# Performance work log

Measured on AMD Instinct MI355X. Metric: run time of the kernel, lower is better.

The kernel has to match this reference:

```python
import jax, jax.numpy as jnp
import numpy as np

EMB = 256
D_INNER = 512                         # expand=2 * d_model
HEADDIM = 64
NHEADS = D_INNER // HEADDIM           # 8
DSTATE = 128
DCONV = 4
CONV_DIM = D_INNER + 2 * DSTATE       # 768 (ngroups=1)
D_IN_PROJ = 2 * D_INNER + 2 * DSTATE + NHEADS  # 1288
LN_EPS = 1e-5


def _layernorm(x, w, b):
    m = jnp.mean(x, axis=-1, keepdims=True)
    v = jnp.mean((x - m) ** 2, axis=-1, keepdims=True)
    return (x - m) * jax.lax.rsqrt(v + LN_EPS) * w + b


def _wn_linear(x, g, v, b):
    # torch weight_norm(dim=0): w = g * v / ||v|| per output row
    w = g[:, None] * v / jnp.linalg.norm(v, axis=1, keepdims=True)
    return x @ w.T + b


def _ssm_scan(x, dt, A, Bm, Cm):
    # x: (b,l,h,p)  dt: (b,l,h)  A: (h,)  Bm/Cm: (b,l,n)
    dA = jnp.exp(dt * A)           # (b,l,h), A<0 so dA in (0,1)
    dtx = dt[..., None] * x        # (b,l,h,p)
    bsz = x.shape[0]

    def step(h, inp):
        dA_t, dtx_t, B_t, C_t = inp
        h = h * dA_t[:, :, None, None] + dtx_t[..., None] * B_t[:, None, None, :]
        y = jnp.einsum('bhpn,bn->bhp', h, C_t)
        return h, y

    h0 = jnp.zeros((bsz, NHEADS, HEADDIM, DSTATE), x.dtype)
    xs = (jnp.swapaxes(dA, 0, 1), jnp.swapaxes(dtx, 0, 1),
          jnp.swapaxes(Bm, 0, 1), jnp.swapaxes(Cm, 0, 1))
    _, ys = jax.lax.scan(step, h0, xs)
    return jnp.swapaxes(ys, 0, 1)  # (b,l,h,p)


def _mamba2(u, in_proj_w, conv_w, conv_b, dt_bias, A_log, D_param, ssm_norm_w, out_proj_w):
    B, L, _ = u.shape
    zxbcdt = u @ in_proj_w.T                       # (B,L,1288)
    z_gate = zxbcdt[..., :D_INNER]
    xBC = zxbcdt[..., D_INNER:D_INNER + CONV_DIM]
    dt = zxbcdt[..., D_INNER + CONV_DIM:]
    # causal depthwise conv1d
    xp = jnp.pad(xBC, ((0, 0), (DCONV - 1, 0), (0, 0)))
    xc = jax.lax.conv_general_dilated(
        jnp.swapaxes(xp, 1, 2), conv_w[:, None, :], (1,), 'VALID',
        feature_group_count=CONV_DIM, dimension_numbers=('NCH', 'OIH', 'NCH'))
    xc = jax.nn.silu(jnp.swapaxes(xc, 1, 2) + conv_b)
    x = xc[..., :D_INNER].reshape(B, L, NHEADS, HEADDIM)
    Bm = xc[..., D_INNER:D_INNER + DSTATE]
    Cm = xc[..., D_INNER + DSTATE:]
    dt = jax.nn.softplus(dt + dt_bias)             # (B,L,H)
    A = -jnp.exp(A_log)                            # (H,)
    y = _ssm_scan(x, dt, A, Bm, Cm) + D_param[None, None, :, None] * x
    y = y.reshape(B, L, D_INNER)
    # gated RMSNorm (norm_before_gate=False): rmsnorm(y * silu(z)) * w
    yg = y * jax.nn.silu(z_gate)
    yn = yg * jax.lax.rsqrt(jnp.mean(yg ** 2, axis=-1, keepdims=True) + LN_EPS) * ssm_norm_w
    return yn @ out_proj_w.T


def setup_inputs() -> dict:
    key = jax.random.key(0)
    ks = jax.random.split(key, 12)
    B, NU, NA = 1, 64, 512

    def rn(k, shape, scale):
        return jax.random.normal(k, shape, dtype=jnp.float32) * scale

    z = rn(ks[0], (B, NU, NA, EMB), 1.0)
    in_proj_w = rn(ks[1], (D_IN_PROJ, EMB), EMB ** -0.5)
    conv_w = rn(ks[2], (CONV_DIM, DCONV), DCONV ** -0.5)
    conv_b = rn(ks[3], (CONV_DIM,), 0.02)
    dt_bias = jnp.log(jnp.expm1(jax.random.uniform(ks[4], (NHEADS,), minval=0.001, maxval=0.1)))
    A_log = jnp.log(jax.random.uniform(ks[5], (NHEADS,), minval=1.0, maxval=16.0))
    D_param = jnp.ones((NHEADS,), dtype=jnp.float32)
    ssm_norm_w = jnp.ones((D_INNER,), dtype=jnp.float32)
    out_proj_w = rn(ks[6], (EMB, D_INNER), D_INNER ** -0.5)
    ff_v = rn(ks[7], (EMB, EMB), EMB ** -0.5)
    ff_g = jnp.linalg.norm(ff_v, axis=1)
    ff_b = jnp.zeros((EMB,), dtype=jnp.float32)
    fc1_v = rn(ks[8], (EMB, EMB), EMB ** -0.5)
    fc1_g = jnp.linalg.norm(fc1_v, axis=1)
    fc1_b = jnp.zeros((EMB,), dtype=jnp.float32)
    fc2_v = rn(ks[9], (EMB, EMB), EMB ** -0.5)
    fc2_g = jnp.linalg.norm(fc2_v, axis=1)
    fc2_b = jnp.zeros((EMB,), dtype=jnp.float32)
    return {
        'z': z,
        'ln1_w': jnp.ones((EMB,), dtype=jnp.float32), 'ln1_b': jnp.zeros((EMB,), dtype=jnp.float32),
        'in_proj_w': in_proj_w, 'conv_w': conv_w, 'conv_b': conv_b,
        'dt_bias': dt_bias, 'A_log': A_log, 'D_param': D_param,
        'ssm_norm_w': ssm_norm_w, 'out_proj_w': out_proj_w,
        'ff_g': ff_g, 'ff_v': ff_v, 'ff_b': ff_b,
        'ln2_w': jnp.ones((EMB,), dtype=jnp.float32), 'ln2_b': jnp.zeros((EMB,), dtype=jnp.float32),
        'fc1_g': fc1_g, 'fc1_v': fc1_v, 'fc1_b': fc1_b,
        'fc2_g': fc2_g, 'fc2_v': fc2_v, 'fc2_b': fc2_b,
    }


def reference(z, ln1_w, ln1_b, in_proj_w, conv_w, conv_b, dt_bias, A_log, D_param,
              ssm_norm_w, out_proj_w, ff_g, ff_v, ff_b, ln2_w, ln2_b,
              fc1_g, fc1_v, fc1_b, fc2_g, fc2_v, fc2_b):
    b, nu, na, e = z.shape
    # MambaBlock: z + ff(mamba(norm(z)))
    u = _layernorm(z, ln1_w, ln1_b).reshape(-1, na, e)
    y = _mamba2(u, in_proj_w, conv_w, conv_b, dt_bias, A_log, D_param, ssm_norm_w, out_proj_w)
    y = _wn_linear(y, ff_g, ff_v, ff_b).reshape(b, nu, na, e)
    z = z + y
    # NormFF: z + Lin2(GELU(Lin1(LN(z))))  (dropout inactive in eval)
    h = _layernorm(z, ln2_w, ln2_b)
    h = jax.nn.gelu(_wn_linear(h, fc1_g, fc1_v, fc1_b), approximate=False)
    h = _wn_linear(h, fc2_g, fc2_v, fc2_b)
    return z + h
```

## Files before the change

### kernel.cpp

```cpp
#include <hip/hip_runtime.h>
#include <stdint.h>
#include <math.h>

#define EMB       256
#define D_INNER   512
#define HEADDIM   64
#define NHEADS    8
#define DSTATE    128
#define DCONV     4
#define CONV_DIM  768
#define LN_EPS    1e-5f
#define NBATCH    64
#define SEQLEN    512
#define NTOK      (NBATCH*SEQLEN)

typedef __attribute__((ext_vector_type(8))) short          short8;
typedef __attribute__((ext_vector_type(8))) unsigned short u16x8;
typedef __attribute__((ext_vector_type(4))) unsigned short u16x4;
typedef __attribute__((ext_vector_type(4))) float          f32x4;

__device__ __forceinline__ float bfb(unsigned short u) {
    union { unsigned int i; float f; } x; x.i = ((unsigned int)u) << 16; return x.f;
}
__device__ __forceinline__ unsigned short fbf(float f) {
    union { float f; unsigned int i; } x; x.f = f;
    unsigned int i = x.i;
    unsigned int lsb = (i >> 16) & 1u;
    i += 0x7fffu + lsb;
    return (unsigned short)(i >> 16);
}

__device__ __forceinline__ void gld16(const unsigned short* g, unsigned short* l) {
    __builtin_amdgcn_global_load_lds((const __attribute__((address_space(1))) void*)g,
                                     (__attribute__((address_space(3))) void*)l, 16, 0, 0);
}

__global__ __launch_bounds__(256) void cvt2_k(const float* __restrict__ a, unsigned short* __restrict__ oa, int na,
                                              const float* __restrict__ b, unsigned short* __restrict__ ob, int nb) {
    int i = blockIdx.x * 256 + threadIdx.x;
    if (i < na) oa[i] = fbf(a[i]);
    else { i -= na; if (i < nb) ob[i] = fbf(b[i]); }
}

__global__ __launch_bounds__(256) void wnorm3_k(const float* __restrict__ g0, const float* __restrict__ v0, unsigned short* __restrict__ o0,
                                                const float* __restrict__ g1, const float* __restrict__ v1, unsigned short* __restrict__ o1,
                                                const float* __restrict__ g2, const float* __restrict__ v2, unsigned short* __restrict__ o2) {
    int o = blockIdx.x & 255, s = blockIdx.x >> 8, tid = threadIdx.x;
    const float* g = s == 0 ? g0 : (s == 1 ? g1 : g2);
    const float* v = s == 0 ? v0 : (s == 1 ? v1 : v2);
    unsigned short* wout = s == 0 ? o0 : (s == 1 ? o1 : o2);
    float x = v[(size_t)o * 256 + tid];
    float q = x * x;
    __shared__ float sm[4];
    #pragma unroll
    for (int d = 32; d; d >>= 1) q += __shfl_down(q, d);
    if ((tid & 63) == 0) sm[tid >> 6] = q;
    __syncthreads();
    float tot = sm[0] + sm[1] + sm[2] + sm[3];
    float scale = g[o] * rsqrtf(tot);
    wout[(size_t)o * 256 + tid] = fbf(x * scale);
}

__global__ __launch_bounds__(256) void wco_k(const unsigned short* __restrict__ wff,
                                             const unsigned short* __restrict__ outWb,
                                             unsigned short* __restrict__ wco) {
    int i = blockIdx.x, tid = threadIdx.x;
    __shared__ float row[256];
    row[tid] = bfb(wff[(size_t)i * 256 + tid]);
    __syncthreads();
    #pragma unroll
    for (int half = 0; half < 2; half++) {
        int k = tid + half * 256;
        float acc = 0.f;
        for (int j = 0; j < 256; j++)
            acc += row[j] * bfb(outWb[(size_t)j * 512 + k]);
        wco[(size_t)i * 512 + k] = fbf(acc);
    }
}

__global__ __launch_bounds__(256) void ln_k(const float* __restrict__ in,
                                            const float* __restrict__ w,
                                            const float* __restrict__ b,
                                            unsigned short* __restrict__ out) {
    int tok = blockIdx.x, tid = threadIdx.x;
    size_t idx = (size_t)tok * 256 + tid;
    float x = in[idx];
    __shared__ float sm[8];
    float s = x;
    #pragma unroll
    for (int o = 32; o; o >>= 1) s += __shfl_down(s, o);
    if ((tid & 63) == 0) sm[tid >> 6] = s;
    __syncthreads();
    float mean = (sm[0] + sm[1] + sm[2] + sm[3]) * (1.f / 256.f);
    float d = x - mean;
    float q = d * d;
    #pragma unroll
    for (int o = 32; o; o >>= 1) q += __shfl_down(q, o);
    if ((tid & 63) == 0) sm[4 + (tid >> 6)] = q;
    __syncthreads();
    float var = (sm[4] + sm[5] + sm[6] + sm[7]) * (1.f / 256.f);
    out[idx] = fbf(d * rsqrtf(var + LN_EPS) * w[tid] + b[tid]);
}

#define BMT 128
#define BNT 128
#define BKT 32
template<int EPI, int NBN>
__global__ __launch_bounds__(256) void gemm_k(const unsigned short* __restrict__ A,
                                              const unsigned short* __restrict__ Bw,
                                              int K, int N,
                                              unsigned short* __restrict__ out_b,
                                              float* __restrict__ out_f,
                                              const float* __restrict__ bias,
                                              const float* __restrict__ res_f,
                                              unsigned short* __restrict__ out2_b) {
    __shared__ __align__(16) unsigned short smem[16384];
    int tid = threadIdx.x;
    int d = blockIdx.x;
    const int cpx = (256 * NBN) >> 3;
    int logical = (d & 7) * cpx + (d >> 3);
    int bm = logical / NBN;
    int bn = logical % NBN;
    int lane = tid & 63, w = tid >> 6;
    int wr = w >> 1, wc = w & 1;
    int fr = lane & 15, fq = lane >> 4;

    int rsub = w * 16 + (lane >> 2);
    int cl   = ((lane & 3) ^ ((rsub >> 1) & 3)) << 3;
    const unsigned short* gA0 = A  + (size_t)(bm * BMT + rsub)      * K + cl;
    const unsigned short* gA1 = A  + (size_t)(bm * BMT + rsub + 64) * K + cl;
    const unsigned short* gB0 = Bw + (size_t)(bn * BNT + rsub)      * K + cl;
    const unsigned short* gB1 = Bw + (size_t)(bn * BNT + rsub + 64) * K + cl;

    f32x4 acc[4][4];
    #pragma unroll
    for (int m = 0; m < 4; m++)
        #pragma unroll
        for (int n = 0; n < 4; n++)
            #pragma unroll
            for (int r = 0; r < 4; r++) acc[m][n][r] = 0.f;

    auto AS = [&](int buf) { return &smem[buf * 4096]; };
    auto BS = [&](int buf) { return &smem[8192 + buf * 4096]; };
    auto STAGE = [&](int buf, int k0) {
        gld16(gA0 + k0, AS(buf) + w * 512);
        gld16(gA1 + k0, AS(buf) + 2048 + w * 512);
        gld16(gB0 + k0, BS(buf) + w * 512);
        gld16(gB1 + k0, BS(buf) + 2048 + w * 512);
    };

    int nt = K / BKT;
    STAGE(0, 0);
    STAGE(1, BKT);
    for (int t = 0; t < nt; ++t) {
        int buf = t & 1;
        if (t < nt - 1) asm volatile("s_waitcnt vmcnt(4)" ::: "memory");
        else            asm volatile("s_waitcnt vmcnt(0)" ::: "memory");
        __builtin_amdgcn_s_barrier();
        short8 af[4], bf_[4];
        #pragma unroll
        for (int m = 0; m < 4; m++) {
            int ra = wr * 64 + m * 16 + fr;
            af[m] = *(const short8*)&AS(buf)[ra * 32 + ((fq ^ ((ra >> 1) & 3)) << 3)];
        }
        #pragma unroll
        for (int n = 0; n < 4; n++) {
            int rb = wc * 64 + n * 16 + fr;
            bf_[n] = *(const short8*)&BS(buf)[rb * 32 + ((fq ^ ((rb >> 1) & 3)) << 3)];
        }
        asm volatile("s_waitcnt lgkmcnt(0)" ::: "memory");
        __builtin_amdgcn_sched_barrier(0);
        __builtin_amdgcn_s_barrier();
        if (t + 2 < nt) STAGE(buf, (t + 2) * BKT);
        __builtin_amdgcn_s_setprio(1);
        #pragma unroll
        for (int m = 0; m < 4; m++)
            #pragma unroll
            for (int n = 0; n < 4; n++)
                acc[m][n] = __builtin_amdgcn_mfma_f32_16x16x32_bf16(af[m], bf_[n], acc[m][n], 0, 0, 0);
        __builtin_amdgcn_s_setprio(0);
    }
    __builtin_amdgcn_s_barrier();

    if (EPI == 1 && bn == 10) {
        #pragma unroll
        for (int m = 0; m < 4; m++)
            #pragma unroll
            for (int n = 0; n < 4; n++)
                #pragma unroll
                for (int r = 0; r < 4; r++) {
                    int grow = bm * BMT + wr * 64 + m * 16 + fq * 4 + r;
                    int gcol = 1280 + wc * 64 + n * 16 + fr;
                    if (gcol < 1288) {
                        float a2 = acc[m][n][r] + bias[gcol - 1280];
                        out_f[(size_t)grow * 8 + (gcol - 1280)] =
                            a2 > 20.f ? a2 : log1pf(expf(a2));
                    }
                }
    } else if (EPI == 0 || EPI == 1) {
        unsigned short* cb = smem;
        #pragma unroll
        for (int s = 0; s < 2; s++) {
            if (wr == s) {
                #pragma unroll
                for (int m = 0; m < 4; m++)
                    #pragma unroll
                    for (int n = 0; n < 4; n++)
                        #pragma unroll
                        for (int r = 0; r < 4; r++)
                            cb[(m * 16 + fq * 4 + r) * 136 + wc * 64 + n * 16 + fr] =
                                fbf(acc[m][n][r]);
            }
            __syncthreads();
            #pragma unroll
            for (int k = 0; k < 4; k++) {
                int g = k * 256 + tid;
                int row = g >> 4, col = (g & 15) << 3;
                u16x8 v = *(const u16x8*)&cb[row * 136 + col];
                int grow = bm * BMT + s * 64 + row;
                int gc = bn * BNT + col;
                if (EPI == 0) {
                    *(u16x8*)&out_b[(size_t)grow * N + gc] = v;
                } else {
                    if (gc < 512) *(u16x8*)&out_b[(size_t)grow * 512 + gc] = v;
                    else          *(u16x8*)&out2_b[(size_t)grow * 768 + (gc - 512)] = v;
                }
            }
            __syncthreads();
        }
    } else {
        float* fb = (float*)smem;
        #pragma unroll
        for (int s = 0; s < 4; s++) {
            if (wr == (s >> 1)) {
                int mp = s & 1;
                #pragma unroll
                for (int mm = 0; mm < 2; mm++)
                    #pragma unroll
                    for (int n = 0; n < 4; n++)
                        #pragma unroll
                        for (int r = 0; r < 4; r++)
                            fb[(mm * 16 + fq * 4 + r) * 132 + wc * 64 + n * 16 + fr] =
                                acc[mp * 2 + mm][n][r];
            }
            __syncthreads();
            #pragma unroll
            for (int k = 0; k < 4; k++) {
                int g = k * 256 + tid;
                int row = g >> 5, col = (g & 31) << 2;
                f32x4 v = *(const f32x4*)&fb[row * 132 + col];
                int grow = bm * BMT + (s >> 1) * 64 + (s & 1) * 32 + row;
                int gc = bn * BNT + col;
                size_t idx = (size_t)grow * 256 + gc;
                if (EPI == 2) {
                    f32x4 rr = *(const f32x4*)&res_f[idx];
                    f32x4 o;
                    #pragma unroll
                    for (int j = 0; j < 4; j++) o[j] = rr[j] + v[j] + bias[gc + j];
                    *(f32x4*)&out_f[idx] = o;
                } else {
                    u16x4 o;
                    #pragma unroll
                    for (int j = 0; j < 4; j++) {
                        float x = v[j] + bias[gc + j];
                        o[j] = fbf(0.5f * x * (1.f + erff(x * 0.70710678118654752f)));
                    }
                    *(u16x4*)&out_b[idx] = o;
                }
            }
            __syncthreads();
        }
    }
}

__global__ __launch_bounds__(256) void conv_k(unsigned short* xbc,
                                              const float* __restrict__ cw,
                                              const float* __restrict__ cb) {
    int b = blockIdx.y;
    int c0 = blockIdx.x * 64;
    int tid = threadIdx.x;
    int c = tid & 63;
    int rq = tid >> 6;
    __shared__ unsigned short sraw[131][72];
    int ca = c0 + c;
    float w0 = cw[ca * 4 + 0], w1 = cw[ca * 4 + 1];
    float w2 = cw[ca * 4 + 2], w3 = cw[ca * 4 + 3];
    float bias = cb[ca];
    unsigned short carry_u = 0;

    for (int t0 = 0; t0 < 512; t0 += 128) {
        __syncthreads();
        if (tid < 192) sraw[rq][c] = carry_u;
        for (int idx = tid; idx < 1024; idx += 256) {
            int lt = idx >> 3, cg = idx & 7;
            *(u16x8*)&sraw[3 + lt][cg * 8] =
                *(const u16x8*)&xbc[((size_t)(b * 512 + t0 + lt)) * 768 + c0 + cg * 8];
        }
        __syncthreads();
        if (tid < 192) carry_u = sraw[128 + rq][c];
        #pragma unroll 4
        for (int i = 0; i < 32; i++) {
            int lt = rq + 4 * i;
            float acc = bias
                + bfb(sraw[lt + 0][c]) * w0
                + bfb(sraw[lt + 1][c]) * w1
                + bfb(sraw[lt + 2][c]) * w2
                + bfb(sraw[lt + 3][c]) * w3;
            acc = acc / (1.f + expf(-acc));
            xbc[((size_t)(b * 512 + t0 + lt)) * 768 + c0 + c] = fbf(acc);
        }
    }
}

#define CPAD 136
#define TPAD 56
#define TOFF(r) ((((r) >> 4) & 3) << 3)
__global__ __launch_bounds__(256) void ssd_k(const unsigned short* __restrict__ xc,
                                             const float* __restrict__ dts,
                                             const float* __restrict__ A_log,
                                             const float* __restrict__ D_param,
                                             unsigned short* __restrict__ y) {
    __shared__ unsigned short Ct[32][CPAD];
    __shared__ unsigned short Bt[32][CPAD];
    __shared__ unsigned short BtT[128][TPAD];
    __shared__ unsigned short DXT[64][TPAD];
    __shared__ unsigned short LG[32][40];
    __shared__ unsigned short hB[64][CPAD];
    __shared__ unsigned short Yb[32][72];
    __shared__ float scum[32], sdt2[32], sEC[32];
    __shared__ float sET[32][36];

    int bh = blockIdx.x;
    int b = bh >> 3, h = bh & 7;
    int tid = threadIdx.x;
    int w = tid >> 6;
    int lane = tid & 63;
    int fr = lane & 15, fq = lane >> 4;

    float A_h = -expf(A_log[h]);
    float D_h = D_param[h];

    f32x4 hacc[8];
    #pragma unroll
    for (int nf = 0; nf < 8; nf++)
        #pragma unroll
        for (int r = 0; r < 4; r++) hacc[nf][r] = 0.f;

    int t  = tid >> 3;
    int e8 = tid & 7;

    for (int c = 0; c < 16; ++c) {
        size_t tok0 = (size_t)b * 512 + c * 32;
        u16x8 bv0, bv1, cv0, cv1, xv;
        {
            const unsigned short* row = &xc[(tok0 + t) * 768];
            bv0 = *(const u16x8*)&row[512 + e8 * 16];
            bv1 = *(const u16x8*)&row[512 + e8 * 16 + 8];
            cv0 = *(const u16x8*)&row[640 + e8 * 16];
            cv1 = *(const u16x8*)&row[640 + e8 * 16 + 8];
            xv  = *(const u16x8*)&row[h * 64 + e8 * 8];
        }
        *(u16x8*)&Ct[t][e8 * 16]     = cv0;
        *(u16x8*)&Ct[t][e8 * 16 + 8] = cv1;
        *(u16x8*)&Bt[t][e8 * 16]     = bv0;
        *(u16x8*)&Bt[t][e8 * 16 + 8] = bv1;
        if (tid < 32) {
            float dtv = dts[(tok0 + tid) * 8 + h];
            sdt2[tid] = dtv;
            float la = dtv * A_h;
            #pragma unroll
            for (int dd = 1; dd < 32; dd <<= 1) {
                float up = __shfl_up(la, dd);
                if (lane >= dd) la += up;
            }
            scum[tid] = la;
        }
        __syncthreads();
        float cumQ = scum[31];
        if (tid < 32) sEC[tid] = expf(scum[tid]);
        {
            float dtv = sdt2[t];
            float wgt = expf(cumQ - scum[t]);
            int tof = TOFF(e8 * 16);
            #pragma unroll
            for (int j = 0; j < 8; j++) {
                float dtx = dtv * bfb(xv[j]);
                int rr = e8 * 8 + j;
                DXT[rr][t + TOFF(rr)] = fbf(dtx);
                BtT[e8 * 16 + j][t + tof]     = fbf(wgt * bfb(bv0[j]));
                BtT[e8 * 16 + 8 + j][t + tof] = fbf(wgt * bfb(bv1[j]));
            }
        }
        #pragma unroll
        for (int k = 0; k < 4; k++) {
            int idx = tid * 4 + k;
            int tt = idx >> 5, tq = idx & 31;
            sET[tt][tq] = (tq <= tt) ? expf(scum[tt] - scum[tq]) : 0.f;
        }
        #pragma unroll
        for (int nf = 0; nf < 8; nf++)
            #pragma unroll
            for (int r = 0; r < 4; r++)
                hB[w * 16 + fq * 4 + r][nf * 16 + fr] = fbf(hacc[nf][r]);
        __syncthreads();
        {
            int m = w >> 1, nf = w & 1;
            f32x4 g;
            #pragma unroll
            for (int r = 0; r < 4; r++) g[r] = 0.f;
            #pragma unroll
            for (int ks = 0; ks < 4; ks++) {
                short8 ca = *(const short8*)&Ct[m * 16 + fr][ks * 32 + fq * 8];
                short8 bb = *(const short8*)&Bt[nf * 16 + fr][ks * 32 + fq * 8];
                g = __builtin_amdgcn_mfma_f32_16x16x32_bf16(ca, bb, g, 0, 0, 0);
            }
            #pragma unroll
            for (int r = 0; r < 4; r++) {
                int tt = m * 16 + fq * 4 + r;
                int tq = nf * 16 + fr;
                LG[tt][tq] = fbf(g[r] * sET[tt][tq]);
            }
        }
        __syncthreads();
        f32x4 Yi[2];
        #pragma unroll
        for (int m = 0; m < 2; m++)
            #pragma unroll
            for (int r = 0; r < 4; r++) Yi[m][r] = 0.f;
        #pragma unroll
        for (int ks = 0; ks < 4; ks++) {
            short8 a0 = *(const short8*)&Ct[fr][ks * 32 + fq * 8];
            short8 a1 = *(const short8*)&Ct[16 + fr][ks * 32 + fq * 8];
            short8 hb = *(const short8*)&hB[w * 16 + fr][ks * 32 + fq * 8];
            Yi[0] = __builtin_amdgcn_mfma_f32_16x16x32_bf16(a0, hb, Yi[0], 0, 0, 0);
            Yi[1] = __builtin_amdgcn_mfma_f32_16x16x32_bf16(a1, hb, Yi[1], 0, 0, 0);
        }
        #pragma unroll
        for (int m = 0; m < 2; m++)
            #pragma unroll
            for (int r = 0; r < 4; r++) Yi[m][r] *= sEC[m * 16 + fq * 4 + r];
        {
            int wof = TOFF(w * 16);
            short8 a0 = *(const short8*)&LG[fr][fq * 8];
            short8 a1 = *(const short8*)&LG[16 + fr][fq * 8];
            short8 dx = *(const short8*)&DXT[w * 16 + fr][fq * 8 + wof];
            Yi[0] = __builtin_amdgcn_mfma_f32_16x16x32_bf16(a0, dx, Yi[0], 0, 0, 0);
            Yi[1] = __builtin_amdgcn_mfma_f32_16x16x32_bf16(a1, dx, Yi[1], 0, 0, 0);
        }
        {
            float ecq = sEC[31];
            #pragma unroll
            for (int nf = 0; nf < 8; nf++)
                #pragma unroll
                for (int r = 0; r < 4; r++) hacc[nf][r] *= ecq;
            int wof = TOFF(w * 16);
            short8 ax = *(const short8*)&DXT[w * 16 + fr][fq * 8 + wof];
            #pragma unroll
            for (int nf = 0; nf < 8; nf++) {
                short8 bb = *(const short8*)&BtT[nf * 16 + fr][fq * 8 + TOFF(nf * 16)];
                hacc[nf] = __builtin_amdgcn_mfma_f32_16x16x32_bf16(ax, bb, hacc[nf], 0, 0, 0);
            }
        }
        #pragma unroll
        for (int m = 0; m < 2; m++)
            #pragma unroll
            for (int r = 0; r < 4; r++) {
                int tt = m * 16 + fq * 4 + r;
                Yb[tt][w * 16 + fr] = fbf(Yi[m][r]);
            }
        __syncthreads();
        {
            u16x8 yv = *(const u16x8*)&Yb[t][e8 * 8];
            u16x8 ov;
            #pragma unroll
            for (int j = 0; j < 8; j++)
                ov[j] = fbf(bfb(yv[j]) + D_h * bfb(xv[j]));
            *(u16x8*)&y[(tok0 + t) * 512 + h * 64 + e8 * 8] = ov;
        }
    }
}

__global__ __launch_bounds__(256) void gate_k(const unsigned short* __restrict__ y,
                                              const unsigned short* __restrict__ zg,
                                              const float* __restrict__ nw,
                                              unsigned short* __restrict__ yn) {
    int tok = blockIdx.x, tid = threadIdx.x;
    size_t base = (size_t)tok * 512;
    float gv[2];
    float q = 0.f;
    #pragma unroll
    for (int j = 0; j < 2; j++) {
        int c = tid + j * 256;
        float yy = bfb(y[base + c]);
        float zz = bfb(zg[base + c]);
        float s = zz / (1.f + expf(-zz));
        float t = yy * s;
        gv[j] = t;
        q += t * t;
    }
    __shared__ float sm[4];
    #pragma unroll
    for (int o = 32; o; o >>= 1) q += __shfl_down(q, o);
    if ((tid & 63) == 0) sm[tid >> 6] = q;
    __syncthreads();
    float ms = (sm[0] + sm[1] + sm[2] + sm[3]) * (1.f / 512.f);
    float r = rsqrtf(ms + LN_EPS);
    #pragma unroll
    for (int j = 0; j < 2; j++) {
        int c = tid + j * 256;
        yn[base + c] = fbf(gv[j] * r * nw[c]);
    }
}

extern "C" void kernel_launch(void* const* d_in, const int* in_sizes, int n_in,
                              void* d_out, int out_size, void* d_ws, size_t ws_size,
                              hipStream_t stream) {
    if (n_in < 22) return;
    static const int setup_sizes[22] = {8388608,256,256,329728,3072,768,8,8,8,512,
                                        131072,256,65536,256,256,256,256,65536,256,256,65536,256};
    for (int i = 0; i < 22; i++) if (in_sizes[i] != setup_sizes[i]) return;

    const float* z      = (const float*)d_in[0];
    const float* ln1w   = (const float*)d_in[1];
    const float* ln1b   = (const float*)d_in[2];
    const float* inW    = (const float*)d_in[3];
    const float* convw  = (const float*)d_in[4];
    const float* convb  = (const float*)d_in[5];
    const float* dtb    = (const float*)d_in[6];
    const float* Alog   = (const float*)d_in[7];
    const float* Dp     = (const float*)d_in[8];
    const float* normw  = (const float*)d_in[9];
    const float* outW   = (const float*)d_in[10];
    const float* ffg    = (const float*)d_in[11];
    const float* ffv    = (const float*)d_in[12];
    const float* ffb    = (const float*)d_in[13];
    const float* ln2w   = (const float*)d_in[14];
    const float* ln2b   = (const float*)d_in[15];
    const float* fc1g   = (const float*)d_in[16];
    const float* fc1v   = (const float*)d_in[17];
    const float* fc1b   = (const float*)d_in[18];
    const float* fc2g   = (const float*)d_in[19];
    const float* fc2v   = (const float*)d_in[20];
    const float* fc2b   = (const float*)d_in[21];
    float* out = (float*)d_out;
    (void)out_size;

    char* ws = (char*)d_ws;
    const size_t SLOT_A = (size_t)NTOK * 768 * 2;
    const size_t SLOT_B = (size_t)NTOK * 512 * 2;
    const size_t SLOT_C = (size_t)NTOK * 512 * 2;
    const size_t SLOT_D = (size_t)NTOK * 256 * 2;
    const size_t SLOT_E = (size_t)NTOK * 8 * 4;
    const size_t SLOT_W = (size_t)256 * 256 * 2;
    const size_t SLOT_WI = (size_t)1288 * 256 * 2;
    const size_t SLOT_WO = (size_t)256 * 512 * 2;
    const size_t SLOT_WC = (size_t)256 * 512 * 2;
    char* pA = ws;
    char* pB = pA + SLOT_A;
    char* pC = pB + SLOT_B;
    char* pD = pC + SLOT_C;
    char* pE = pD + SLOT_D;
    char* pW = pE + SLOT_E;
    char* pWI = pW + 3 * SLOT_W;
    char* pWO = pWI + SLOT_WI;
    char* pWC = pWO + SLOT_WO;
    size_t need = SLOT_A + SLOT_B + SLOT_C + SLOT_D + SLOT_E + 3 * SLOT_W + SLOT_WI + SLOT_WO + SLOT_WC;
    if (ws_size < need) return;

    unsigned short* xbc = (unsigned short*)pA;
    unsigned short* yn  = (unsigned short*)pA;
    unsigned short* t2  = (unsigned short*)(pA + (size_t)NTOK * 512 * 2);
    unsigned short* y   = (unsigned short*)pB;
    float*          z2  = (float*)pB;
    unsigned short* zgb = (unsigned short*)pC;
    unsigned short* u   = (unsigned short*)pD;
    unsigned short* h1  = (unsigned short*)pD;
    float*          dts = (float*)pE;
    unsigned short* wff  = (unsigned short*)pW;
    unsigned short* wfc1 = (unsigned short*)(pW + SLOT_W);
    unsigned short* wfc2 = (unsigned short*)(pW + 2 * SLOT_W);
    unsigned short* inWb = (unsigned short*)pWI;
    unsigned short* outWb = (unsigned short*)pWO;
    unsigned short* wco  = (unsigned short*)pWC;

    cvt2_k<<<(1288 * 256 + 131072 + 255) / 256, 256, 0, stream>>>(inW, inWb, 1288 * 256,
                                                                  outW, outWb, 131072);
    wnorm3_k<<<768, 256, 0, stream>>>(ffg, ffv, wff, fc1g, fc1v, wfc1, fc2g, fc2v, wfc2);
    wco_k<<<256, 256, 0, stream>>>(wff, outWb, wco);
    ln_k<<<NTOK, 256, 0, stream>>>(z, ln1w, ln1b, u);
    gemm_k<1, 11><<<256 * 11, 256, 0, stream>>>(u, inWb, 256, 1288,
                                                zgb, dts, dtb, nullptr, xbc);
    conv_k<<<dim3(12, 64), 256, 0, stream>>>(xbc, convw, convb);
    ssd_k<<<NBATCH * NHEADS, 256, 0, stream>>>(xbc, dts, Alog, Dp, y);
    gate_k<<<NTOK, 256, 0, stream>>>(y, zgb, normw, yn);
    gemm_k<2, 2><<<256 * 2, 256, 0, stream>>>(yn, wco, 512, 256,
                                              nullptr, z2, ffb, z, nullptr);
    ln_k<<<NTOK, 256, 0, stream>>>(z2, ln2w, ln2b, t2);
    gemm_k<3, 2><<<256 * 2, 256, 0, stream>>>(t2, wfc1, 256, 256,
                                              h1, nullptr, fc1b, nullptr, nullptr);
    gemm_k<2, 2><<<256 * 2, 256, 0, stream>>>(h1, wfc2, 256, 256,
                                              nullptr, out, fc2b, z2, nullptr);
}
```

Before: 317.6 us.

## Parallelize causal conv over time chunks using halo rows written by in-proj GEMM

The in-projection GEMM epilogue now also writes the last three pre-conv rows of each 128-token chunk into a separate halo buffer. This lets the conv kernel run each chunk independently, with a 3D grid of 4 chunks per batch instead of a serial carry loop over time, which raises parallelism fourfold. The GEMM also takes K as a compile-time template parameter so the loop count is constant, and its launch bounds request 3 waves per SIMD for occupancy. The cost is extra workspace, extra conditional stores in the GEMM epilogue, and a small extra halo read in the conv.

Result: slower. 336.8 us (+6.0%).

```diff
diff --git a/kernel.cpp b/kernel.cpp
--- a/kernel.cpp
+++ b/kernel.cpp
@@ -105,15 +105,16 @@
 #define BMT 128
 #define BNT 128
 #define BKT 32
-template<int EPI, int NBN>
-__global__ __launch_bounds__(256) void gemm_k(const unsigned short* __restrict__ A,
-                                              const unsigned short* __restrict__ Bw,
-                                              int K, int N,
-                                              unsigned short* __restrict__ out_b,
-                                              float* __restrict__ out_f,
-                                              const float* __restrict__ bias,
-                                              const float* __restrict__ res_f,
-                                              unsigned short* __restrict__ out2_b) {
+template<int EPI, int NBN, int KT>
+__global__ __launch_bounds__(256, 3) void gemm_k(const unsigned short* __restrict__ A,
+                                                 const unsigned short* __restrict__ Bw,
+                                                 int N,
+                                                 unsigned short* __restrict__ out_b,
+                                                 float* __restrict__ out_f,
+                                                 const float* __restrict__ bias,
+                                                 const float* __restrict__ res_f,
+                                                 unsigned short* __restrict__ out2_b,
+                                                 unsigned short* __restrict__ halo) {
     __shared__ __align__(16) unsigned short smem[16384];
     int tid = threadIdx.x;
     int d = blockIdx.x;
@@ -127,10 +128,8 @@
 
     int rsub = w * 16 + (lane >> 2);
     int cl   = ((lane & 3) ^ ((rsub >> 1) & 3)) << 3;
-    const unsigned short* gA0 = A  + (size_t)(bm * BMT + rsub)      * K + cl;
-    const unsigned short* gA1 = A  + (size_t)(bm * BMT + rsub + 64) * K + cl;
-    const unsigned short* gB0 = Bw + (size_t)(bn * BNT + rsub)      * K + cl;
-    const unsigned short* gB1 = Bw + (size_t)(bn * BNT + rsub + 64) * K + cl;
+    const unsigned short* gA0 = A  + (size_t)(bm * BMT + rsub) * KT + cl;
+    const unsigned short* gB0 = Bw + (size_t)(bn * BNT + rsub) * KT + cl;
 
     f32x4 acc[4][4];
     #pragma unroll
@@ -144,12 +143,12 @@
     auto BS = [&](int buf) { return &smem[8192 + buf * 4096]; };
     auto STAGE = [&](int buf, int k0) {
         gld16(gA0 + k0, AS(buf) + w * 512);
-        gld16(gA1 + k0, AS(buf) + 2048 + w * 512);
+        gld16(gA0 + k0 + (size_t)64 * KT, AS(buf) + 2048 + w * 512);
         gld16(gB0 + k0, BS(buf) + w * 512);
-        gld16(gB1 + k0, BS(buf) + 2048 + w * 512);
+        gld16(gB0 + k0 + (size_t)64 * KT, BS(buf) + 2048 + w * 512);
     };
 
-    int nt = K / BKT;
+    constexpr int nt = KT / BKT;
     STAGE(0, 0);
     STAGE(1, BKT);
     for (int t = 0; t < nt; ++t) {
@@ -223,7 +222,13 @@
                     *(u16x8*)&out_b[(size_t)grow * N + gc] = v;
                 } else {
                     if (gc < 512) *(u16x8*)&out_b[(size_t)grow * 512 + gc] = v;
-                    else          *(u16x8*)&out2_b[(size_t)grow * 768 + (gc - 512)] = v;
+                    else {
+                        *(u16x8*)&out2_b[(size_t)grow * 768 + (gc - 512)] = v;
+                        int tr = grow & 127;
+                        int H  = grow >> 7;
+                        if (tr >= 125 && (H & 3) != 3)
+                            *(u16x8*)&halo[((size_t)(H + 1) * 3 + (tr - 125)) * 768 + (gc - 512)] = v;
+                    }
                 }
             }
             __syncthreads();
@@ -274,41 +279,44 @@
 }
 
 __global__ __launch_bounds__(256) void conv_k(unsigned short* xbc,
+                                              const unsigned short* __restrict__ halo,
                                               const float* __restrict__ cw,
                                               const float* __restrict__ cb) {
-    int b = blockIdx.y;
+    int b  = blockIdx.y;
+    int c  = blockIdx.z;
     int c0 = blockIdx.x * 64;
+    int t0 = c * 128;
     int tid = threadIdx.x;
-    int c = tid & 63;
-    int rq = tid >> 6;
+    int cth = tid & 63;
+    int rq  = tid >> 6;
     __shared__ unsigned short sraw[131][72];
-    int ca = c0 + c;
+
+    int ca = c0 + cth;
     float w0 = cw[ca * 4 + 0], w1 = cw[ca * 4 + 1];
     float w2 = cw[ca * 4 + 2], w3 = cw[ca * 4 + 3];
     float bias = cb[ca];
-    unsigned short carry_u = 0;
-
-    for (int t0 = 0; t0 < 512; t0 += 128) {
-        __syncthreads();
-        if (tid < 192) sraw[rq][c] = carry_u;
-        for (int idx = tid; idx < 1024; idx += 256) {
-            int lt = idx >> 3, cg = idx & 7;
-            *(u16x8*)&sraw[3 + lt][cg * 8] =
-                *(const u16x8*)&xbc[((size_t)(b * 512 + t0 + lt)) * 768 + c0 + cg * 8];
-        }
-        __syncthreads();
-        if (tid < 192) carry_u = sraw[128 + rq][c];
-        #pragma unroll 4
-        for (int i = 0; i < 32; i++) {
-            int lt = rq + 4 * i;
-            float acc = bias
-                + bfb(sraw[lt + 0][c]) * w0
-                + bfb(sraw[lt + 1][c]) * w1
-                + bfb(sraw[lt + 2][c]) * w2
-                + bfb(sraw[lt + 3][c]) * w3;
-            acc = acc / (1.f + expf(-acc));
-            xbc[((size_t)(b * 512 + t0 + lt)) * 768 + c0 + c] = fbf(acc);
-        }
+
+    if (tid < 192) {
+        int j = tid >> 6, cc = tid & 63;
+        sraw[j][cc] = (c == 0) ? (unsigned short)0
+            : halo[((size_t)(b * 4 + c) * 3 + j) * 768 + c0 + cc];
+    }
+    for (int idx = tid; idx < 1024; idx += 256) {
+        int lt = idx >> 3, cg = idx & 7;
+        *(u16x8*)&sraw[3 + lt][cg * 8] =
+            *(const u16x8*)&xbc[((size_t)(b * 512 + t0 + lt)) * 768 + c0 + cg * 8];
+    }
+    __syncthreads();
+    #pragma unroll 4
+    for (int i = 0; i < 32; i++) {
+        int lt = rq + 4 * i;
+        float acc = bias
+            + bfb(sraw[lt + 0][cth]) * w0
+            + bfb(sraw[lt + 1][cth]) * w1
+            + bfb(sraw[lt + 2][cth]) * w2
+            + bfb(sraw[lt + 3][cth]) * w3;
+        acc = acc / (1.f + expf(-acc));
+        xbc[((size_t)(b * 512 + t0 + lt)) * 768 + c0 + cth] = fbf(acc);
     }
 }
 
@@ -555,6 +563,7 @@
     const size_t SLOT_WI = (size_t)1288 * 256 * 2;
     const size_t SLOT_WO = (size_t)256 * 512 * 2;
     const size_t SLOT_WC = (size_t)256 * 512 * 2;
+    const size_t SLOT_H  = (size_t)256 * 3 * 768 * 2;
     char* pA = ws;
     char* pB = pA + SLOT_A;
     char* pC = pB + SLOT_B;
@@ -564,7 +573,8 @@
     char* pWI = pW + 3 * SLOT_W;
     char* pWO = pWI + SLOT_WI;
     char* pWC = pWO + SLOT_WO;
-    size_t need = SLOT_A + SLOT_B + SLOT_C + SLOT_D + SLOT_E + 3 * SLOT_W + SLOT_WI + SLOT_WO + SLOT_WC;
+    char* pH  = pWC + SLOT_WC;
+    size_t need = SLOT_A + SLOT_B + SLOT_C + SLOT_D + SLOT_E + 3 * SLOT_W + SLOT_WI + SLOT_WO + SLOT_WC + SLOT_H;
     if (ws_size < need) return;
 
     unsigned short* xbc = (unsigned short*)pA;
@@ -582,22 +592,23 @@
     unsigned short* inWb = (unsigned short*)pWI;
     unsigned short* outWb = (unsigned short*)pWO;
     unsigned short* wco  = (unsigned short*)pWC;
+    unsigned short* halo = (unsigned short*)pH;
 
     cvt2_k<<<(1288 * 256 + 131072 + 255) / 256, 256, 0, stream>>>(inW, inWb, 1288 * 256,
                                                                   outW, outWb, 131072);
     wnorm3_k<<<768, 256, 0, stream>>>(ffg, ffv, wff, fc1g, fc1v, wfc1, fc2g, fc2v, wfc2);
     wco_k<<<256, 256, 0, stream>>>(wff, outWb, wco);
     ln_k<<<NTOK, 256, 0, stream>>>(z, ln1w, ln1b, u);
-    gemm_k<1, 11><<<256 * 11, 256, 0, stream>>>(u, inWb, 256, 1288,
-                                                zgb, dts, dtb, nullptr, xbc);
-    conv_k<<<dim3(12, 64), 256, 0, stream>>>(xbc, convw, convb);
+    gemm_k<1, 11, 256><<<256 * 11, 256, 0, stream>>>(u, inWb, 1288,
+                                                     zgb, dts, dtb, nullptr, xbc, halo);
+    conv_k<<<dim3(12, 64, 4), 256, 0, stream>>>(xbc, halo, convw, convb);
     ssd_k<<<NBATCH * NHEADS, 256, 0, stream>>>(xbc, dts, Alog, Dp, y);
     gate_k<<<NTOK, 256, 0, stream>>>(y, zgb, normw, yn);
-    gemm_k<2, 2><<<256 * 2, 256, 0, stream>>>(yn, wco, 512, 256,
-                                              nullptr, z2, ffb, z, nullptr);
+    gemm_k<2, 2, 512><<<256 * 2, 256, 0, stream>>>(yn, wco, 256,
+                                                   nullptr, z2, ffb, z, nullptr, nullptr);
     ln_k<<<NTOK, 256, 0, stream>>>(z2, ln2w, ln2b, t2);
-    gemm_k<3, 2><<<256 * 2, 256, 0, stream>>>(t2, wfc1, 256, 256,
-                                              h1, nullptr, fc1b, nullptr, nullptr);
-    gemm_k<2, 2><<<256 * 2, 256, 0, stream>>>(h1, wfc2, 256, 256,
-                                              nullptr, out, fc2b, z2, nullptr);
-}
+    gemm_k<3, 2, 256><<<256 * 2, 256, 0, stream>>>(t2, wfc1, 256,
+                                                   h1, nullptr, fc1b, nullptr, nullptr, nullptr);
+    gemm_k<2, 2, 256><<<256 * 2, 256, 0, stream>>>(h1, wfc2, 256,
+                                                   nullptr, out, fc2b, z2, nullptr, nullptr);
+}
```

## Split causal conv across time chunks with halo buffer; prefetch SSD inputs

Applied to the files above, without the earlier changes.

A new halo kernel copies the three boundary rows before each 128-token chunk into a side buffer. The conv kernel can then run one block per chunk, giving 4x more blocks instead of a serial loop over chunks per block. The SSD kernel remaps block indices so that heads of the same batch group are spread across blocks, and it prefetches the next chunk's B/C/x rows into registers before the barrier to hide global load latency. The cost is an extra kernel launch, more workspace, and higher register pressure in ssd_k.

Measured after the change: 308.6 us. -2.8%, faster.

```diff
diff --git a/kernel.cpp b/kernel.cpp
--- a/kernel.cpp
+++ b/kernel.cpp
@@ -273,42 +273,58 @@
     }
 }
 
+__global__ __launch_bounds__(256) void halo_k(const unsigned short* __restrict__ xbc,
+                                              unsigned short* __restrict__ halo) {
+    int blk = blockIdx.x;
+    int b = blk / 3, c = blk % 3 + 1;
+    int tid = threadIdx.x;
+    for (int i = tid; i < 288; i += 256) {
+        int j = i / 96, off = (i % 96) * 8;
+        size_t tok = (size_t)b * 512 + c * 128 - 3 + j;
+        *(u16x8*)&halo[((size_t)(b * 4 + c) * 3 + j) * 768 + off] =
+            *(const u16x8*)&xbc[tok * 768 + off];
+    }
+}
+
 __global__ __launch_bounds__(256) void conv_k(unsigned short* xbc,
+                                              const unsigned short* __restrict__ halo,
                                               const float* __restrict__ cw,
                                               const float* __restrict__ cb) {
-    int b = blockIdx.y;
+    int b  = blockIdx.y;
+    int c  = blockIdx.z;
     int c0 = blockIdx.x * 64;
+    int t0 = c * 128;
     int tid = threadIdx.x;
-    int c = tid & 63;
-    int rq = tid >> 6;
+    int cth = tid & 63;
+    int rq  = tid >> 6;
     __shared__ unsigned short sraw[131][72];
-    int ca = c0 + c;
+
+    int ca = c0 + cth;
     float w0 = cw[ca * 4 + 0], w1 = cw[ca * 4 + 1];
     float w2 = cw[ca * 4 + 2], w3 = cw[ca * 4 + 3];
     float bias = cb[ca];
-    unsigned short carry_u = 0;
-
-    for (int t0 = 0; t0 < 512; t0 += 128) {
-        __syncthreads();
-        if (tid < 192) sraw[rq][c] = carry_u;
-        for (int idx = tid; idx < 1024; idx += 256) {
-            int lt = idx >> 3, cg = idx & 7;
-            *(u16x8*)&sraw[3 + lt][cg * 8] =
-                *(const u16x8*)&xbc[((size_t)(b * 512 + t0 + lt)) * 768 + c0 + cg * 8];
-        }
-        __syncthreads();
-        if (tid < 192) carry_u = sraw[128 + rq][c];
-        #pragma unroll 4
-        for (int i = 0; i < 32; i++) {
-            int lt = rq + 4 * i;
-            float acc = bias
-                + bfb(sraw[lt + 0][c]) * w0
-                + bfb(sraw[lt + 1][c]) * w1
-                + bfb(sraw[lt + 2][c]) * w2
-                + bfb(sraw[lt + 3][c]) * w3;
-            acc = acc / (1.f + expf(-acc));
-            xbc[((size_t)(b * 512 + t0 + lt)) * 768 + c0 + c] = fbf(acc);
-        }
+
+    if (tid < 192) {
+        int j = tid >> 6, cc = tid & 63;
+        sraw[j][cc] = (c == 0) ? (unsigned short)0
+            : halo[((size_t)(b * 4 + c) * 3 + j) * 768 + c0 + cc];
+    }
+    for (int idx = tid; idx < 1024; idx += 256) {
+        int lt = idx >> 3, cg = idx & 7;
+        *(u16x8*)&sraw[3 + lt][cg * 8] =
+            *(const u16x8*)&xbc[((size_t)(b * 512 + t0 + lt)) * 768 + c0 + cg * 8];
+    }
+    __syncthreads();
+    #pragma unroll 4
+    for (int i = 0; i < 32; i++) {
+        int lt = rq + 4 * i;
+        float acc = bias
+            + bfb(sraw[lt + 0][cth]) * w0
+            + bfb(sraw[lt + 1][cth]) * w1
+            + bfb(sraw[lt + 2][cth]) * w2
+            + bfb(sraw[lt + 3][cth]) * w3;
+        acc = acc / (1.f + expf(-acc));
+        xbc[((size_t)(b * 512 + t0 + lt)) * 768 + c0 + cth] = fbf(acc);
     }
 }
 
@@ -330,8 +346,9 @@
     __shared__ float scum[32], sdt2[32], sEC[32];
     __shared__ float sET[32][36];
 
-    int bh = blockIdx.x;
-    int b = bh >> 3, h = bh & 7;
+    int d = blockIdx.x;
+    int b = (d & 7) | (((d >> 6) & 7) << 3);
+    int h = (d >> 3) & 7;
     int tid = threadIdx.x;
     int w = tid >> 6;
     int lane = tid & 63;
@@ -349,17 +366,18 @@
     int t  = tid >> 3;
     int e8 = tid & 7;
 
+    u16x8 bv0, bv1, cv0, cv1, xv;
+    {
+        const unsigned short* row = &xc[((size_t)b * 512 + t) * 768];
+        bv0 = *(const u16x8*)&row[512 + e8 * 16];
+        bv1 = *(const u16x8*)&row[512 + e8 * 16 + 8];
+        cv0 = *(const u16x8*)&row[640 + e8 * 16];
+        cv1 = *(const u16x8*)&row[640 + e8 * 16 + 8];
+        xv  = *(const u16x8*)&row[h * 64 + e8 * 8];
+    }
+
     for (int c = 0; c < 16; ++c) {
         size_t tok0 = (size_t)b * 512 + c * 32;
-        u16x8 bv0, bv1, cv0, cv1, xv;
-        {
-            const unsigned short* row = &xc[(tok0 + t) * 768];
-            bv0 = *(const u16x8*)&row[512 + e8 * 16];
-            bv1 = *(const u16x8*)&row[512 + e8 * 16 + 8];
-            cv0 = *(const u16x8*)&row[640 + e8 * 16];
-            cv1 = *(const u16x8*)&row[640 + e8 * 16 + 8];
-            xv  = *(const u16x8*)&row[h * 64 + e8 * 8];
-        }
         *(u16x8*)&Ct[t][e8 * 16]     = cv0;
         *(u16x8*)&Ct[t][e8 * 16 + 8] = cv1;
         *(u16x8*)&Bt[t][e8 * 16]     = bv0;
@@ -402,6 +420,16 @@
             #pragma unroll
             for (int r = 0; r < 4; r++)
                 hB[w * 16 + fq * 4 + r][nf * 16 + fr] = fbf(hacc[nf][r]);
+        u16x8 nbv0, nbv1, ncv0, ncv1, nxv;
+        {
+            size_t ptok = (c + 1 < 16) ? (tok0 + 32 + t) : (tok0 + t);
+            const unsigned short* row = &xc[ptok * 768];
+            nbv0 = *(const u16x8*)&row[512 + e8 * 16];
+            nbv1 = *(const u16x8*)&row[512 + e8 * 16 + 8];
+            ncv0 = *(const u16x8*)&row[640 + e8 * 16];
+            ncv1 = *(const u16x8*)&row[640 + e8 * 16 + 8];
+            nxv  = *(const u16x8*)&row[h * 64 + e8 * 8];
+        }
         __syncthreads();
         {
             int m = w >> 1, nf = w & 1;
@@ -477,6 +505,7 @@
                 ov[j] = fbf(bfb(yv[j]) + D_h * bfb(xv[j]));
             *(u16x8*)&y[(tok0 + t) * 512 + h * 64 + e8 * 8] = ov;
         }
+        bv0 = nbv0; bv1 = nbv1; cv0 = ncv0; cv1 = ncv1; xv = nxv;
     }
 }
 
@@ -555,6 +584,7 @@
     const size_t SLOT_WI = (size_t)1288 * 256 * 2;
     const size_t SLOT_WO = (size_t)256 * 512 * 2;
     const size_t SLOT_WC = (size_t)256 * 512 * 2;
+    const size_t SLOT_H  = (size_t)256 * 3 * 768 * 2;
     char* pA = ws;
     char* pB = pA + SLOT_A;
     char* pC = pB + SLOT_B;
@@ -564,7 +594,8 @@
     char* pWI = pW + 3 * SLOT_W;
     char* pWO = pWI + SLOT_WI;
     char* pWC = pWO + SLOT_WO;
-    size_t need = SLOT_A + SLOT_B + SLOT_C + SLOT_D + SLOT_E + 3 * SLOT_W + SLOT_WI + SLOT_WO + SLOT_WC;
+    char* pH  = pWC + SLOT_WC;
+    size_t need = SLOT_A + SLOT_B + SLOT_C + SLOT_D + SLOT_E + 3 * SLOT_W + SLOT_WI + SLOT_WO + SLOT_WC + SLOT_H;
     if (ws_size < need) return;
 
     unsigned short* xbc = (unsigned short*)pA;
@@ -582,6 +613,7 @@
     unsigned short* inWb = (unsigned short*)pWI;
     unsigned short* outWb = (unsigned short*)pWO;
     unsigned short* wco  = (unsigned short*)pWC;
+    unsigned short* halo = (unsigned short*)pH;
 
     cvt2_k<<<(1288 * 256 + 131072 + 255) / 256, 256, 0, stream>>>(inW, inWb, 1288 * 256,
                                                                   outW, outWb, 131072);
@@ -590,7 +622,8 @@
     ln_k<<<NTOK, 256, 0, stream>>>(z, ln1w, ln1b, u);
     gemm_k<1, 11><<<256 * 11, 256, 0, stream>>>(u, inWb, 256, 1288,
                                                 zgb, dts, dtb, nullptr, xbc);
-    conv_k<<<dim3(12, 64), 256, 0, stream>>>(xbc, convw, convb);
+    halo_k<<<192, 256, 0, stream>>>(xbc, halo);
+    conv_k<<<dim3(12, 64, 4), 256, 0, stream>>>(xbc, halo, convw, convb);
     ssd_k<<<NBATCH * NHEADS, 256, 0, stream>>>(xbc, dts, Alog, Dp, y);
     gate_k<<<NTOK, 256, 0, stream>>>(y, zgb, normw, yn);
     gemm_k<2, 2><<<256 * 2, 256, 0, stream>>>(yn, wco, 512, 256,
```
